# Kernel tuning notes

Measured on AMD Instinct MI355X. Metric: run time of the kernel, lower is better.

Reference implementation:

```python
import jax, jax.numpy as jnp
import numpy as np

N_SRC = 50000; N_DST = 50000; E = 800000
IN_NODE = 128; IN_EDGE = 16; OUT_NODE = 64; OUT_EDGE = 16; H = 4
LEAKY_SLOPE = 0.01  # F.leaky_relu default used inside dgl EGATConv


def setup_inputs() -> dict:
    key = jax.random.key(0)
    ks = jax.random.split(key, 11)
    return dict(
        nfeats=jax.random.normal(ks[0], (N_SRC, IN_NODE), jnp.float32),
        dst_feats=jax.random.normal(ks[1], (N_DST, IN_NODE), jnp.float32),
        reward=jax.random.uniform(ks[2], (E,), jnp.float32),
        src=jax.random.randint(ks[3], (E,), 0, N_SRC),
        dst=jax.random.randint(ks[4], (E,), 0, N_DST),
        W_ns=jax.random.normal(ks[5], (IN_NODE, H * OUT_NODE), jnp.float32) * 0.05,
        b_ns=jnp.zeros((H * OUT_NODE,), jnp.float32),
        W_ni=jax.random.normal(ks[6], (IN_NODE, H * OUT_EDGE), jnp.float32) * 0.05,
        W_nj=jax.random.normal(ks[7], (IN_NODE, H * OUT_EDGE), jnp.float32) * 0.05,
        W_fij=jax.random.normal(ks[8], (IN_EDGE, H * OUT_EDGE), jnp.float32) * 0.05,
        attn=jax.random.normal(ks[9], (H, OUT_EDGE), jnp.float32) * 0.05,
        b_e=jnp.zeros((H * OUT_EDGE,), jnp.float32),
    )


def reference(nfeats, dst_feats, reward, src, dst,
              W_ns, b_ns, W_ni, W_nj, W_fij, attn, b_e):
    # EGAT.forward with num_layers=1: efeats = reward repeated to IN_EDGE cols
    efeats = jnp.repeat(reward[:, None], IN_EDGE, axis=1)              # (E, Fe_in)
    # --- EGATConv ---
    f_ni = nfeats @ W_ni                                               # (Ns, H*Fe)
    f_nj = dst_feats @ W_nj                                            # (Nd, H*Fe)
    f_out = f_ni[src] + f_nj[dst] + efeats @ W_fij + b_e               # (E, H*Fe)
    f_out = jax.nn.leaky_relu(f_out, LEAKY_SLOPE).reshape(E, H, OUT_EDGE)
    e = jnp.einsum('ehf,hf->eh', f_out, attn)                          # (E, H)
    # edge softmax over incoming edges of each dst node (stable)
    m = jax.ops.segment_max(e, dst, num_segments=N_DST)                # (Nd, H)
    a = jnp.exp(e - m[dst])
    s = jax.ops.segment_sum(a, dst, num_segments=N_DST)                # (Nd, H)
    a = a / jnp.where(s > 0, s, 1.0)[dst]                              # (E, H)
    # weighted aggregation of projected src features
    h_src = (nfeats @ W_ns + b_ns).reshape(N_SRC, H, OUT_NODE)
    msg = h_src[src] * a[:, :, None]                                   # (E, H, Fn)
    h_out = jax.ops.segment_sum(msg, dst, num_segments=N_DST)          # (Nd, H, Fn)
    # wrapper: mean over heads then ReLU
    return jax.nn.relu(h_out.mean(axis=1))                             # (Nd, Fn)
```

## Files before the change

kernel.cpp:

```cpp
#include <hip/hip_runtime.h>

#define IN_NODE 128
#define OUT_NODE 64
#define NHEAD 4
#define HN 256
#define HE 64
#define LEAKY 0.01f

typedef __attribute__((ext_vector_type(8))) short bf16x8;
typedef __attribute__((ext_vector_type(4))) float f32x4;

__device__ __forceinline__ float bf2f(unsigned short u) {
    union { unsigned u; float f; } v; v.u = ((unsigned)u) << 16; return v.f;
}
__device__ __forceinline__ unsigned short f2bf(float x) {
    union { float f; unsigned u; } v; v.f = x;
    unsigned r = v.u + 0x7FFF + ((v.u >> 16) & 1);
    return (unsigned short)(r >> 16);
}
__device__ __forceinline__ bf16x8 cvt8(float4 a, float4 b) {
    bf16x8 r;
    r[0] = (short)f2bf(a.x); r[1] = (short)f2bf(a.y);
    r[2] = (short)f2bf(a.z); r[3] = (short)f2bf(a.w);
    r[4] = (short)f2bf(b.x); r[5] = (short)f2bf(b.y);
    r[6] = (short)f2bf(b.z); r[7] = (short)f2bf(b.w);
    return r;
}

__global__ void prep_hist(const float* __restrict__ W_fij,
                          const float* __restrict__ W_ni,
                          const float* __restrict__ W_ns,
                          const float* __restrict__ W_nj,
                          const int* __restrict__ dst,
                          float* __restrict__ wsum, unsigned short* __restrict__ WT,
                          int* __restrict__ cnt, int E) {
    int b = blockIdx.x;
    if (b == 0) {
        int k = threadIdx.x;
        if (k < 64) {
            float s = 0.f;
#pragma unroll
            for (int c = 0; c < 16; ++c) s += W_fij[c * 64 + k];
            wsum[k] = s;
        }
        return;
    }
    if (b <= 12) {
        int base = (b - 1) * 4096 + threadIdx.x;
#pragma unroll
        for (int i = 0; i < 16; ++i) {
            int idx = base + i * 256;
            int g   = idx >> 11;
            int rem = idx & 2047;
            int c   = rem >> 9;
            int l   = (rem >> 3) & 63;
            int j   = rem & 7;
            int nl  = l & 15;
            int k   = c * 32 + (l >> 4) * 8 + j;
            unsigned short v;
            if (g < 4)       v = f2bf(W_ni[k * 64  + g * 16 + nl]);
            else if (g < 20) v = f2bf(W_ns[k * 256 + (g - 4) * 16 + nl]);
            else             v = f2bf(W_nj[k * 64  + (g - 20) * 16 + nl]);
            WT[idx] = v;
        }
        return;
    }
    int i = (b - 13) * 256 + threadIdx.x;
    if (i < E) atomicAdd(&cnt[dst[i]], 1);
}

__global__ __launch_bounds__(256) void scan_all(const int* __restrict__ cnt,
                                                int* __restrict__ row_ptr,
                                                int* __restrict__ partials,
                                                int* __restrict__ flags,
                                                int n, int E, int nb) {
    __shared__ int sums[256];
    __shared__ int s_base;
    int tid = threadIdx.x, b = blockIdx.x;
    int base = b * 1024;
    int v[4]; int tsum = 0;
#pragma unroll
    for (int j = 0; j < 4; ++j) {
        int idx = base + tid * 4 + j;
        v[j] = (idx < n) ? cnt[idx] : 0;
        tsum += v[j];
    }
    sums[tid] = tsum;
    __syncthreads();
    for (int off = 1; off < 256; off <<= 1) {
        int x = (tid >= off) ? sums[tid - off] : 0;
        __syncthreads();
        sums[tid] += x;
        __syncthreads();
    }
    if (tid == 255) {
        __hip_atomic_store(&partials[b], sums[255], __ATOMIC_RELAXED, __HIP_MEMORY_SCOPE_AGENT);
        __hip_atomic_store(&flags[b], 1, __ATOMIC_RELEASE, __HIP_MEMORY_SCOPE_AGENT);
    }
    if (tid < 64) {
        int val = 0;
        if (tid < nb) {
            while (__hip_atomic_load(&flags[tid], __ATOMIC_ACQUIRE, __HIP_MEMORY_SCOPE_AGENT) == 0) {
                __builtin_amdgcn_s_sleep(1);
            }
            val = __hip_atomic_load(&partials[tid], __ATOMIC_RELAXED, __HIP_MEMORY_SCOPE_AGENT);
        }
#pragma unroll
        for (int o = 1; o < 64; o <<= 1) {
            int x = __shfl_up(val, o);
            if (tid >= o) val += x;
        }
        int off = (b > 0) ? __shfl(val, b - 1) : 0;
        if (tid == 0) s_base = off;
    }
    __syncthreads();
    int run = s_base + sums[tid] - tsum;
#pragma unroll
    for (int j = 0; j < 4; ++j) {
        int idx = base + tid * 4 + j;
        if (idx < n) row_ptr[idx] = run;
        run += v[j];
    }
    if (b == nb - 1 && tid == 0) row_ptr[n] = E;
}

template<int NG, int G0>
__device__ __forceinline__ void gemm_tile(
    const float* __restrict__ A, int rowBase, int M,
    const unsigned short* __restrict__ WB, const float* __restrict__ b_ns,
    unsigned short* __restrict__ f_ni, unsigned short* __restrict__ h_src,
    unsigned short* __restrict__ f_nj, unsigned short* As)
{
    const int t = threadIdx.x;
    const float4* A4 = reinterpret_cast<const float4*>(A);
#pragma unroll
    for (int j = 0; j < 4; ++j) {
        int gi = j * 256 + t;
        int r  = gi >> 4;
        int gr = rowBase + r; if (gr >= M) gr = M - 1;
        int fi = (gi & 15) * 2;
        float4 a0 = A4[(size_t)gr * 32 + fi];
        float4 a1 = A4[(size_t)gr * 32 + fi + 1];
        int byteoff = (gi * 16) ^ ((r & 7) << 4);
        *reinterpret_cast<bf16x8*>(reinterpret_cast<char*>(As) + byteoff) = cvt8(a0, a1);
    }
    __syncthreads();

    const int lane = t & 63, w = t >> 6;
    const int rw = rowBase + w * 16;
    if (rw >= M) return;
    const int m = lane & 15, q = lane >> 4;
    const int tr = w * 16 + m;

    f32x4 acc[NG] = {};
    const char* Asb = reinterpret_cast<const char*>(As);
#pragma unroll
    for (int c = 0; c < 4; ++c) {
        int gi  = tr * 16 + c * 4 + q;
        int off = (gi * 16) ^ ((tr & 7) << 4);
        bf16x8 af = *reinterpret_cast<const bf16x8*>(Asb + off);
#pragma unroll
        for (int g = 0; g < NG; ++g) {
            bf16x8 bf = *reinterpret_cast<const bf16x8*>(
                WB + (size_t)(((G0 + g) * 4 + c) * 64 + lane) * 8);
            acc[g] = __builtin_amdgcn_mfma_f32_16x16x32_bf16(af, bf, acc[g], 0, 0, 0);
        }
    }

#pragma unroll
    for (int g = 0; g < NG; ++g) {
        const int ga = G0 + g;
        unsigned short* C; int N, colBase; const float* bias = nullptr;
        if (ga < 4)       { C = f_ni;  N = 64;  colBase = ga * 16; }
        else if (ga < 20) { C = h_src; N = 256; colBase = (ga - 4) * 16; bias = b_ns; }
        else              { C = f_nj;  N = 64;  colBase = (ga - 20) * 16; }
        int col = colBase + m;
        float bv = bias ? bias[col] : 0.f;
#pragma unroll
        for (int rr = 0; rr < 4; ++rr) {
            int orow = rw + q * 4 + rr;
            if (orow < M) C[(size_t)orow * N + col] = f2bf(acc[g][rr] + bv);
        }
    }
}

__global__ __launch_bounds__(256) void mega(
    const float* __restrict__ nfeats, const float* __restrict__ dst_feats,
    const unsigned short* __restrict__ WT, const float* __restrict__ b_ns,
    const int* __restrict__ src, const int* __restrict__ dst,
    const float* __restrict__ reward, const int* __restrict__ row_ptr,
    int* __restrict__ cnt,
    unsigned short* __restrict__ f_ni, unsigned short* __restrict__ h_src,
    unsigned short* __restrict__ f_nj, int2* __restrict__ sr_s,
    int Ns, int Nd, int E, int nBlkNf, int nBlkDj, int nScatter)
{
    __shared__ __align__(16) unsigned short As[64 * 128];
    const int g = blockIdx.x / 3, r = blockIdx.x % 3;
    if (r == 0) {
        if (g < nBlkNf) {
            gemm_tile<20, 0>(nfeats, g * 64, Ns, WT, b_ns, f_ni, h_src, f_nj, As);
        } else if (g < nBlkNf + nBlkDj) {
            gemm_tile<4, 20>(dst_feats, (g - nBlkNf) * 64, Nd, WT, b_ns, f_ni, h_src, f_nj, As);
        }
        return;
    }
    const int sb = g * 2 + (r - 1);
    if (sb >= nScatter) return;
    int i = sb * 256 + threadIdx.x;
    if (i >= E) return;
    int d = dst[i];
    int pos = row_ptr[d] + atomicSub(&cnt[d], 1) - 1;
    sr_s[pos] = make_int2(src[i], __float_as_int(reward[i]));
}

__global__ __launch_bounds__(256) void fused_agg(
    const unsigned short* __restrict__ f_ni, const unsigned short* __restrict__ f_nj,
    const unsigned short* __restrict__ h_src, const int2* __restrict__ sr_s,
    const int* __restrict__ row_ptr,
    const float* __restrict__ wsum, const float* __restrict__ b_e,
    const float* __restrict__ attn, float* __restrict__ out, int Nd)
{
    const int wv = threadIdx.x >> 6, lane = threadIdx.x & 63;
    const int d = blockIdx.x * 4 + wv;
    if (d >= Nd) return;
    const int l = lane & 15, sub = lane >> 4;
    const int beg = row_ptr[d];
    const int end = row_ptr[d + 1];
    const int hsel = (lane >> 4) << 2;

    ushort4 uj = *reinterpret_cast<const ushort4*>(f_nj + (size_t)d * HE + 4 * l);
    float4 fnj = { bf2f(uj.x), bf2f(uj.y), bf2f(uj.z), bf2f(uj.w) };
    float4 ws = *reinterpret_cast<const float4*>(wsum + 4 * l);
    float4 be = *reinterpret_cast<const float4*>(b_e + 4 * l);
    float4 at = *reinterpret_cast<const float4*>(attn + 4 * l);

    float den = 0.f;
    float a0 = 0.f, a1 = 0.f, a2 = 0.f, a3 = 0.f;

    const int deg = end - beg;
    const int nfull = deg & ~3;

    for (int base = beg; base < beg + nfull; base += 4) {
        int2 sr = sr_s[base + sub];
        int sn = sr.x;
        float r = __int_as_float(sr.y);
        ushort4 ui = *reinterpret_cast<const ushort4*>(f_ni + (size_t)sn * HE + 4 * l);
        float t, v;
        v = bf2f(ui.x) + fnj.x + r * ws.x + be.x; v = (v >= 0.f) ? v : LEAKY * v; t  = v * at.x;
        v = bf2f(ui.y) + fnj.y + r * ws.y + be.y; v = (v >= 0.f) ? v : LEAKY * v; t += v * at.y;
        v = bf2f(ui.z) + fnj.z + r * ws.z + be.z; v = (v >= 0.f) ? v : LEAKY * v; t += v * at.z;
        v = bf2f(ui.w) + fnj.w + r * ws.w + be.w; v = (v >= 0.f) ? v : LEAKY * v; t += v * at.w;
        t += __shfl_xor(t, 1);
        t += __shfl_xor(t, 2);
        float ev = __expf(t);
        den += ev;
#pragma unroll
        for (int e = 0; e < 4; ++e) {
            float w  = __shfl(ev, e * 16 + hsel);
            int   sa = __shfl(sn, e * 16);
            ushort4 u = *reinterpret_cast<const ushort4*>(h_src + (size_t)sa * HN + lane * 4);
            a0 = fmaf(w, bf2f(u.x), a0);
            a1 = fmaf(w, bf2f(u.y), a1);
            a2 = fmaf(w, bf2f(u.z), a2);
            a3 = fmaf(w, bf2f(u.w), a3);
        }
    }

    const int rem = deg & 3;
    if (rem) {
        int base = beg + nfull;
        int slot = base + sub;
        float ev = 0.f; int sn = 0;
        if (sub < rem) {
            int2 sr = sr_s[slot];
            sn = sr.x;
            float r = __int_as_float(sr.y);
            ushort4 ui = *reinterpret_cast<const ushort4*>(f_ni + (size_t)sn * HE + 4 * l);
            float t, v;
            v = bf2f(ui.x) + fnj.x + r * ws.x + be.x; v = (v >= 0.f) ? v : LEAKY * v; t  = v * at.x;
            v = bf2f(ui.y) + fnj.y + r * ws.y + be.y; v = (v >= 0.f) ? v : LEAKY * v; t += v * at.y;
            v = bf2f(ui.z) + fnj.z + r * ws.z + be.z; v = (v >= 0.f) ? v : LEAKY * v; t += v * at.z;
            v = bf2f(ui.w) + fnj.w + r * ws.w + be.w; v = (v >= 0.f) ? v : LEAKY * v; t += v * at.w;
            t += __shfl_xor(t, 1);
            t += __shfl_xor(t, 2);
            ev = __expf(t);
            den += ev;
        }
        for (int e = 0; e < rem; ++e) {
            float w  = __shfl(ev, e * 16 + hsel);
            int   sa = __shfl(sn, e * 16);
            ushort4 u = *reinterpret_cast<const ushort4*>(h_src + (size_t)sa * HN + lane * 4);
            a0 = fmaf(w, bf2f(u.x), a0);
            a1 = fmaf(w, bf2f(u.y), a1);
            a2 = fmaf(w, bf2f(u.z), a2);
            a3 = fmaf(w, bf2f(u.w), a3);
        }
    }

    den += __shfl_xor(den, 16);
    den += __shfl_xor(den, 32);
    float dh = __shfl(den, hsel);
    float invh = (dh > 0.f) ? 1.f / dh : 0.f;
    a0 *= invh; a1 *= invh; a2 *= invh; a3 *= invh;

    a0 += __shfl_xor(a0, 16); a0 += __shfl_xor(a0, 32);
    a1 += __shfl_xor(a1, 16); a1 += __shfl_xor(a1, 32);
    a2 += __shfl_xor(a2, 16); a2 += __shfl_xor(a2, 32);
    a3 += __shfl_xor(a3, 16); a3 += __shfl_xor(a3, 32);
    if (lane < 16) {
        float4 o = { fmaxf(a0 * 0.25f, 0.f), fmaxf(a1 * 0.25f, 0.f),
                     fmaxf(a2 * 0.25f, 0.f), fmaxf(a3 * 0.25f, 0.f) };
        *reinterpret_cast<float4*>(out + (size_t)d * OUT_NODE + lane * 4) = o;
    }
}

static inline char* align256(char* p) {
    return (char*)(((uintptr_t)p + 255) & ~(uintptr_t)255);
}

extern "C" void kernel_launch(void* const* d_in, const int* in_sizes, int n_in,
                              void* d_out, int out_size, void* d_ws, size_t ws_size,
                              hipStream_t stream) {
    const float* nfeats    = (const float*)d_in[0];
    const float* dst_feats = (const float*)d_in[1];
    const float* reward    = (const float*)d_in[2];
    const int*   src       = (const int*)d_in[3];
    const int*   dst       = (const int*)d_in[4];
    const float* W_ns      = (const float*)d_in[5];
    const float* b_ns      = (const float*)d_in[6];
    const float* W_ni      = (const float*)d_in[7];
    const float* W_nj      = (const float*)d_in[8];
    const float* W_fij     = (const float*)d_in[9];
    const float* attn      = (const float*)d_in[10];
    const float* b_e       = (const float*)d_in[11];
    float* out = (float*)d_out;

    const int Ns = in_sizes[0] / IN_NODE;
    const int Nd = in_sizes[1] / IN_NODE;
    const int E  = in_sizes[2];

    char* ws = (char*)d_ws;
    unsigned short* f_ni  = (unsigned short*)ws; ws = align256(ws + (size_t)Ns * HE * 2);
    unsigned short* f_nj  = (unsigned short*)ws; ws = align256(ws + (size_t)Nd * HE * 2);
    unsigned short* h_src = (unsigned short*)ws; ws = align256(ws + (size_t)Ns * HN * 2);
    unsigned short* WT    = (unsigned short*)ws; ws = align256(ws + 49152 * 2);
    float* wsum    = (float*)ws; ws = align256(ws + HE * 4);
    int*   cnt     = (int*)ws;
    int*   flags   = cnt + Nd;   ws = align256(ws + (size_t)(Nd + 64) * 4);
    int*   row_ptr = (int*)ws;   ws = align256(ws + (size_t)(Nd + 1) * 4);
    int*   partials= (int*)ws;   ws = align256(ws + 256 * 4);
    int2*  sr_s    = (int2*)ws;  ws = align256(ws + (size_t)E * 8);

    hipMemsetAsync(cnt, 0, (size_t)(Nd + 64) * 4, stream);

    prep_hist<<<13 + (E + 255) / 256, 256, 0, stream>>>(
        W_fij, W_ni, W_ns, W_nj, dst, wsum, WT, cnt, E);

    int nb = (Nd + 1023) / 1024;
    scan_all<<<nb, 256, 0, stream>>>(cnt, row_ptr, partials, flags, Nd, E, nb);

    int nBlkNf = (Ns + 63) / 64;
    int nBlkDj = (Nd + 63) / 64;
    int nG = nBlkNf + nBlkDj;
    int nScatter = (E + 255) / 256;
    int nGroups = (nG > (nScatter + 1) / 2) ? nG : (nScatter + 1) / 2;
    mega<<<nGroups * 3, 256, 0, stream>>>(
        nfeats, dst_feats, WT, b_ns, src, dst, reward, row_ptr, cnt,
        f_ni, h_src, f_nj, sr_s, Ns, Nd, E, nBlkNf, nBlkDj, nScatter);

    fused_agg<<<(Nd + 3) / 4, 256, 0, stream>>>(
        f_ni, f_nj, h_src, sr_s, row_ptr, wsum, b_e, attn, out, Nd);
}
```

Measured before the change: 278.1 us.

## Software-pipeline edge gathers and restructure per-edge-group aggregation in fused_agg

Reworks the aggregation loop so each 16-lane group handles its own edge and gathers the full 256-wide h_src row for it, instead of broadcasting each edge's source index across the wave. It also prefetches the next edge's index, f_ni and h_src rows one iteration ahead and folds the remainder edges into the main loop through clamped indices and a validity mask. Softmax normalisation is applied per head at the end. The intent is to hide gather latency and remove the serial shuffle-then-load chain, at the cost of more registers, which may lower occupancy.

Result: no change. 273.0 us (-1.8%).

```diff
diff --git a/kernel.cpp b/kernel.cpp
--- a/kernel.cpp
+++ b/kernel.cpp
@@ -224,92 +224,115 @@
     const int d = blockIdx.x * 4 + wv;
     if (d >= Nd) return;
     const int l = lane & 15, sub = lane >> 4;
+
     const int beg = row_ptr[d];
     const int end = row_ptr[d + 1];
-    const int hsel = (lane >> 4) << 2;
+    const int deg = end - beg;
+
+    if (deg <= 0) {
+        if (lane < 16) {
+            float4 z = {0.f, 0.f, 0.f, 0.f};
+            *reinterpret_cast<float4*>(out + (size_t)d * OUT_NODE + lane * 4) = z;
+        }
+        return;
+    }
 
     ushort4 uj = *reinterpret_cast<const ushort4*>(f_nj + (size_t)d * HE + 4 * l);
-    float4 fnj = { bf2f(uj.x), bf2f(uj.y), bf2f(uj.z), bf2f(uj.w) };
     float4 ws = *reinterpret_cast<const float4*>(wsum + 4 * l);
     float4 be = *reinterpret_cast<const float4*>(b_e + 4 * l);
     float4 at = *reinterpret_cast<const float4*>(attn + 4 * l);
+    float4 bb = { bf2f(uj.x) + be.x, bf2f(uj.y) + be.y,
+                  bf2f(uj.z) + be.z, bf2f(uj.w) + be.w };
+
+    const int nq = (deg + 3) >> 2;
+    const int last = end - 1;
 
     float den = 0.f;
-    float a0 = 0.f, a1 = 0.f, a2 = 0.f, a3 = 0.f;
-
-    const int deg = end - beg;
-    const int nfull = deg & ~3;
-
-    for (int base = beg; base < beg + nfull; base += 4) {
-        int2 sr = sr_s[base + sub];
-        int sn = sr.x;
-        float r = __int_as_float(sr.y);
-        ushort4 ui = *reinterpret_cast<const ushort4*>(f_ni + (size_t)sn * HE + 4 * l);
-        float t, v;
-        v = bf2f(ui.x) + fnj.x + r * ws.x + be.x; v = (v >= 0.f) ? v : LEAKY * v; t  = v * at.x;
-        v = bf2f(ui.y) + fnj.y + r * ws.y + be.y; v = (v >= 0.f) ? v : LEAKY * v; t += v * at.y;
-        v = bf2f(ui.z) + fnj.z + r * ws.z + be.z; v = (v >= 0.f) ? v : LEAKY * v; t += v * at.z;
-        v = bf2f(ui.w) + fnj.w + r * ws.w + be.w; v = (v >= 0.f) ? v : LEAKY * v; t += v * at.w;
+    f32x4 ac0 = {}, ac1 = {}, ac2 = {}, ac3 = {};
+
+#define LDSR(q) ({ int qq = ((q) < nq) ? (q) : (nq - 1);                 \
+                   int slot = beg + qq * 4 + sub;                        \
+                   if (slot > last) slot = last;                         \
+                   sr_s[slot]; })
+
+    int2 srA = LDSR(0);
+    int2 srB = LDSR(1);
+    const unsigned short* pA = f_ni + (size_t)srA.x * HE + 4 * l;
+    ushort4 uiA = *reinterpret_cast<const ushort4*>(pA);
+    const unsigned short* hA = h_src + (size_t)srA.x * HN + 4 * l;
+    ushort4 uA0 = *reinterpret_cast<const ushort4*>(hA);
+    ushort4 uA1 = *reinterpret_cast<const ushort4*>(hA + 64);
+    ushort4 uA2 = *reinterpret_cast<const ushort4*>(hA + 128);
+    ushort4 uA3 = *reinterpret_cast<const ushort4*>(hA + 192);
+
+    for (int k = 0; k < nq; ++k) {
+        int2 srC = LDSR(k + 2);
+        const unsigned short* pB = f_ni + (size_t)srB.x * HE + 4 * l;
+        ushort4 uiB = *reinterpret_cast<const ushort4*>(pB);
+        const unsigned short* hB = h_src + (size_t)srB.x * HN + 4 * l;
+        ushort4 uB0 = *reinterpret_cast<const ushort4*>(hB);
+        ushort4 uB1 = *reinterpret_cast<const ushort4*>(hB + 64);
+        ushort4 uB2 = *reinterpret_cast<const ushort4*>(hB + 128);
+        ushort4 uB3 = *reinterpret_cast<const ushort4*>(hB + 192);
+
+        float r = __int_as_float(srA.y);
+        float v, t;
+        v = bf2f(uiA.x) + fmaf(r, ws.x, bb.x); v = fmaxf(v, LEAKY * v); t  = v * at.x;
+        v = bf2f(uiA.y) + fmaf(r, ws.y, bb.y); v = fmaxf(v, LEAKY * v); t = fmaf(v, at.y, t);
+        v = bf2f(uiA.z) + fmaf(r, ws.z, bb.z); v = fmaxf(v, LEAKY * v); t = fmaf(v, at.z, t);
+        v = bf2f(uiA.w) + fmaf(r, ws.w, bb.w); v = fmaxf(v, LEAKY * v); t = fmaf(v, at.w, t);
         t += __shfl_xor(t, 1);
         t += __shfl_xor(t, 2);
-        float ev = __expf(t);
+        bool valid = (beg + k * 4 + sub) < end;
+        float ev = valid ? __expf(t) : 0.f;
         den += ev;
-#pragma unroll
-        for (int e = 0; e < 4; ++e) {
-            float w  = __shfl(ev, e * 16 + hsel);
-            int   sa = __shfl(sn, e * 16);
-            ushort4 u = *reinterpret_cast<const ushort4*>(h_src + (size_t)sa * HN + lane * 4);
-            a0 = fmaf(w, bf2f(u.x), a0);
-            a1 = fmaf(w, bf2f(u.y), a1);
-            a2 = fmaf(w, bf2f(u.z), a2);
-            a3 = fmaf(w, bf2f(u.w), a3);
-        }
-    }
-
-    const int rem = deg & 3;
-    if (rem) {
-        int base = beg + nfull;
-        int slot = base + sub;
-        float ev = 0.f; int sn = 0;
-        if (sub < rem) {
-            int2 sr = sr_s[slot];
-            sn = sr.x;
-            float r = __int_as_float(sr.y);
-            ushort4 ui = *reinterpret_cast<const ushort4*>(f_ni + (size_t)sn * HE + 4 * l);
-            float t, v;
-            v = bf2f(ui.x) + fnj.x + r * ws.x + be.x; v = (v >= 0.f) ? v : LEAKY * v; t  = v * at.x;
-            v = bf2f(ui.y) + fnj.y + r * ws.y + be.y; v = (v >= 0.f) ? v : LEAKY * v; t += v * at.y;
-            v = bf2f(ui.z) + fnj.z + r * ws.z + be.z; v = (v >= 0.f) ? v : LEAKY * v; t += v * at.z;
-            v = bf2f(ui.w) + fnj.w + r * ws.w + be.w; v = (v >= 0.f) ? v : LEAKY * v; t += v * at.w;
-            t += __shfl_xor(t, 1);
-            t += __shfl_xor(t, 2);
-            ev = __expf(t);
-            den += ev;
-        }
-        for (int e = 0; e < rem; ++e) {
-            float w  = __shfl(ev, e * 16 + hsel);
-            int   sa = __shfl(sn, e * 16);
-            ushort4 u = *reinterpret_cast<const ushort4*>(h_src + (size_t)sa * HN + lane * 4);
-            a0 = fmaf(w, bf2f(u.x), a0);
-            a1 = fmaf(w, bf2f(u.y), a1);
-            a2 = fmaf(w, bf2f(u.z), a2);
-            a3 = fmaf(w, bf2f(u.w), a3);
-        }
-    }
+        float w0 = __shfl(ev, (lane & 48));
+        float w1 = __shfl(ev, (lane & 48) + 4);
+        float w2 = __shfl(ev, (lane & 48) + 8);
+        float w3 = __shfl(ev, (lane & 48) + 12);
+        ac0[0] = fmaf(w0, bf2f(uA0.x), ac0[0]);
+        ac0[1] = fmaf(w0, bf2f(uA0.y), ac0[1]);
+        ac0[2] = fmaf(w0, bf2f(uA0.z), ac0[2]);
+        ac0[3] = fmaf(w0, bf2f(uA0.w), ac0[3]);
+        ac1[0] = fmaf(w1, bf2f(uA1.x), ac1[0]);
+        ac1[1] = fmaf(w1, bf2f(uA1.y), ac1[1]);
+        ac1[2] = fmaf(w1, bf2f(uA1.z), ac1[2]);
+        ac1[3] = fmaf(w1, bf2f(uA1.w), ac1[3]);
+        ac2[0] = fmaf(w2, bf2f(uA2.x), ac2[0]);
+        ac2[1] = fmaf(w2, bf2f(uA2.y), ac2[1]);
+        ac2[2] = fmaf(w2, bf2f(uA2.z), ac2[2]);
+        ac2[3] = fmaf(w2, bf2f(uA2.w), ac2[3]);
+        ac3[0] = fmaf(w3, bf2f(uA3.x), ac3[0]);
+        ac3[1] = fmaf(w3, bf2f(uA3.y), ac3[1]);
+        ac3[2] = fmaf(w3, bf2f(uA3.z), ac3[2]);
+        ac3[3] = fmaf(w3, bf2f(uA3.w), ac3[3]);
+
+        srA = srB; srB = srC;
+        uiA = uiB;
+        uA0 = uB0; uA1 = uB1; uA2 = uB2; uA3 = uB3;
+    }
+#undef LDSR
 
     den += __shfl_xor(den, 16);
     den += __shfl_xor(den, 32);
-    float dh = __shfl(den, hsel);
-    float invh = (dh > 0.f) ? 1.f / dh : 0.f;
-    a0 *= invh; a1 *= invh; a2 *= invh; a3 *= invh;
-
-    a0 += __shfl_xor(a0, 16); a0 += __shfl_xor(a0, 32);
-    a1 += __shfl_xor(a1, 16); a1 += __shfl_xor(a1, 32);
-    a2 += __shfl_xor(a2, 16); a2 += __shfl_xor(a2, 32);
-    a3 += __shfl_xor(a3, 16); a3 += __shfl_xor(a3, 32);
+    float d0 = __shfl(den, 0), d1 = __shfl(den, 4);
+    float d2 = __shfl(den, 8), d3 = __shfl(den, 12);
+    float i0 = (d0 > 0.f) ? 0.25f / d0 : 0.f;
+    float i1 = (d1 > 0.f) ? 0.25f / d1 : 0.f;
+    float i2 = (d2 > 0.f) ? 0.25f / d2 : 0.f;
+    float i3 = (d3 > 0.f) ? 0.25f / d3 : 0.f;
+
+    float o0 = fmaf(ac3[0], i3, fmaf(ac2[0], i2, fmaf(ac1[0], i1, ac0[0] * i0)));
+    float o1 = fmaf(ac3[1], i3, fmaf(ac2[1], i2, fmaf(ac1[1], i1, ac0[1] * i0)));
+    float o2 = fmaf(ac3[2], i3, fmaf(ac2[2], i2, fmaf(ac1[2], i1, ac0[2] * i0)));
+    float o3 = fmaf(ac3[3], i3, fmaf(ac2[3], i2, fmaf(ac1[3], i1, ac0[3] * i0)));
+    o0 += __shfl_xor(o0, 16); o0 += __shfl_xor(o0, 32);
+    o1 += __shfl_xor(o1, 16); o1 += __shfl_xor(o1, 32);
+    o2 += __shfl_xor(o2, 16); o2 += __shfl_xor(o2, 32);
+    o3 += __shfl_xor(o3, 16); o3 += __shfl_xor(o3, 32);
     if (lane < 16) {
-        float4 o = { fmaxf(a0 * 0.25f, 0.f), fmaxf(a1 * 0.25f, 0.f),
-                     fmaxf(a2 * 0.25f, 0.f), fmaxf(a3 * 0.25f, 0.f) };
+        float4 o = { fmaxf(o0, 0.f), fmaxf(o1, 0.f),
+                     fmaxf(o2, 0.f), fmaxf(o3, 0.f) };
         *reinterpret_cast<float4*>(out + (size_t)d * OUT_NODE + lane * 4) = o;
     }
 }
```

## Restructure edge aggregation with multi-node waves, software-pipelined gathers, and LDS head reduction

Applied to the files above, without the earlier changes.

The fused aggregation kernel now gives each wavefront 8 destination nodes instead of one. Edge gathers are software-pipelined two iterations ahead, and each lane handles a full edge's 16-element h_src slice with wide loads, where before four shuffled per-edge loads were used. Packed float2 math handles the bf16 conversion, leaky-relu and accumulation, and the head and sub-group reduction goes through LDS instead of cross-lane shuffles. The aim is to hide gather latency and cut shuffle and instruction overhead. The cost is more registers, which may lower occupancy, and coarser load balancing across nodes.

Measured after the change: 279.4 us. Within noise of the previous version (+0.5%).

```diff
diff --git a/kernel.cpp b/kernel.cpp
--- a/kernel.cpp
+++ b/kernel.cpp
@@ -6,9 +6,11 @@
 #define HN 256
 #define HE 64
 #define LEAKY 0.01f
+#define DPW 8
 
 typedef __attribute__((ext_vector_type(8))) short bf16x8;
 typedef __attribute__((ext_vector_type(4))) float f32x4;
+typedef __attribute__((ext_vector_type(2))) float f32x2;
 
 __device__ __forceinline__ float bf2f(unsigned short u) {
     union { unsigned u; float f; } v; v.u = ((unsigned)u) << 16; return v.f;
@@ -25,6 +27,11 @@
     r[4] = (short)f2bf(b.x); r[5] = (short)f2bf(b.y);
     r[6] = (short)f2bf(b.z); r[7] = (short)f2bf(b.w);
     return r;
+}
+__device__ __forceinline__ f32x2 bfcvt2(unsigned d) {
+    union { unsigned u; float f; } lo, hi;
+    lo.u = d << 16; hi.u = d & 0xFFFF0000u;
+    f32x2 r; r.x = lo.f; r.y = hi.f; return r;
 }
 
 __global__ void prep_hist(const float* __restrict__ W_fij,
@@ -213,6 +220,18 @@
     sr_s[pos] = make_int2(src[i], __float_as_int(reward[i]));
 }
 
+struct G { uint2 ui; uint4 h0; uint4 h1; };
+__device__ __forceinline__ G gatherE(const unsigned short* __restrict__ f_ni,
+                                     const unsigned short* __restrict__ h_src,
+                                     int sn, int ll, int hq) {
+    G g;
+    g.ui = *reinterpret_cast<const uint2*>(f_ni + (size_t)sn * HE + 4 * ll);
+    const unsigned short* hp = h_src + (size_t)sn * HN + hq;
+    g.h0 = *reinterpret_cast<const uint4*>(hp);
+    g.h1 = *reinterpret_cast<const uint4*>(hp + 8);
+    return g;
+}
+
 __global__ __launch_bounds__(256) void fused_agg(
     const unsigned short* __restrict__ f_ni, const unsigned short* __restrict__ f_nj,
     const unsigned short* __restrict__ h_src, const int2* __restrict__ sr_s,
@@ -220,97 +239,106 @@
     const float* __restrict__ wsum, const float* __restrict__ b_e,
     const float* __restrict__ attn, float* __restrict__ out, int Nd)
 {
+    __shared__ float red[4][1024];
     const int wv = threadIdx.x >> 6, lane = threadIdx.x & 63;
-    const int d = blockIdx.x * 4 + wv;
-    if (d >= Nd) return;
-    const int l = lane & 15, sub = lane >> 4;
-    const int beg = row_ptr[d];
-    const int end = row_ptr[d + 1];
-    const int hsel = (lane >> 4) << 2;
-
-    ushort4 uj = *reinterpret_cast<const ushort4*>(f_nj + (size_t)d * HE + 4 * l);
-    float4 fnj = { bf2f(uj.x), bf2f(uj.y), bf2f(uj.z), bf2f(uj.w) };
-    float4 ws = *reinterpret_cast<const float4*>(wsum + 4 * l);
-    float4 be = *reinterpret_cast<const float4*>(b_e + 4 * l);
-    float4 at = *reinterpret_cast<const float4*>(attn + 4 * l);
-
-    float den = 0.f;
-    float a0 = 0.f, a1 = 0.f, a2 = 0.f, a3 = 0.f;
-
-    const int deg = end - beg;
-    const int nfull = deg & ~3;
-
-    for (int base = beg; base < beg + nfull; base += 4) {
-        int2 sr = sr_s[base + sub];
-        int sn = sr.x;
-        float r = __int_as_float(sr.y);
-        ushort4 ui = *reinterpret_cast<const ushort4*>(f_ni + (size_t)sn * HE + 4 * l);
-        float t, v;
-        v = bf2f(ui.x) + fnj.x + r * ws.x + be.x; v = (v >= 0.f) ? v : LEAKY * v; t  = v * at.x;
-        v = bf2f(ui.y) + fnj.y + r * ws.y + be.y; v = (v >= 0.f) ? v : LEAKY * v; t += v * at.y;
-        v = bf2f(ui.z) + fnj.z + r * ws.z + be.z; v = (v >= 0.f) ? v : LEAKY * v; t += v * at.z;
-        v = bf2f(ui.w) + fnj.w + r * ws.w + be.w; v = (v >= 0.f) ? v : LEAKY * v; t += v * at.w;
-        t += __shfl_xor(t, 1);
-        t += __shfl_xor(t, 2);
-        float ev = __expf(t);
-        den += ev;
-#pragma unroll
-        for (int e = 0; e < 4; ++e) {
-            float w  = __shfl(ev, e * 16 + hsel);
-            int   sa = __shfl(sn, e * 16);
-            ushort4 u = *reinterpret_cast<const ushort4*>(h_src + (size_t)sa * HN + lane * 4);
-            a0 = fmaf(w, bf2f(u.x), a0);
-            a1 = fmaf(w, bf2f(u.y), a1);
-            a2 = fmaf(w, bf2f(u.z), a2);
-            a3 = fmaf(w, bf2f(u.w), a3);
-        }
-    }
-
-    const int rem = deg & 3;
-    if (rem) {
-        int base = beg + nfull;
-        int slot = base + sub;
-        float ev = 0.f; int sn = 0;
-        if (sub < rem) {
-            int2 sr = sr_s[slot];
-            sn = sr.x;
-            float r = __int_as_float(sr.y);
-            ushort4 ui = *reinterpret_cast<const ushort4*>(f_ni + (size_t)sn * HE + 4 * l);
-            float t, v;
-            v = bf2f(ui.x) + fnj.x + r * ws.x + be.x; v = (v >= 0.f) ? v : LEAKY * v; t  = v * at.x;
-            v = bf2f(ui.y) + fnj.y + r * ws.y + be.y; v = (v >= 0.f) ? v : LEAKY * v; t += v * at.y;
-            v = bf2f(ui.z) + fnj.z + r * ws.z + be.z; v = (v >= 0.f) ? v : LEAKY * v; t += v * at.z;
-            v = bf2f(ui.w) + fnj.w + r * ws.w + be.w; v = (v >= 0.f) ? v : LEAKY * v; t += v * at.w;
-            t += __shfl_xor(t, 1);
-            t += __shfl_xor(t, 2);
-            ev = __expf(t);
-            den += ev;
-        }
-        for (int e = 0; e < rem; ++e) {
-            float w  = __shfl(ev, e * 16 + hsel);
-            int   sa = __shfl(sn, e * 16);
-            ushort4 u = *reinterpret_cast<const ushort4*>(h_src + (size_t)sa * HN + lane * 4);
-            a0 = fmaf(w, bf2f(u.x), a0);
-            a1 = fmaf(w, bf2f(u.y), a1);
-            a2 = fmaf(w, bf2f(u.z), a2);
-            a3 = fmaf(w, bf2f(u.w), a3);
-        }
-    }
-
-    den += __shfl_xor(den, 16);
-    den += __shfl_xor(den, 32);
-    float dh = __shfl(den, hsel);
-    float invh = (dh > 0.f) ? 1.f / dh : 0.f;
-    a0 *= invh; a1 *= invh; a2 *= invh; a3 *= invh;
-
-    a0 += __shfl_xor(a0, 16); a0 += __shfl_xor(a0, 32);
-    a1 += __shfl_xor(a1, 16); a1 += __shfl_xor(a1, 32);
-    a2 += __shfl_xor(a2, 16); a2 += __shfl_xor(a2, 32);
-    a3 += __shfl_xor(a3, 16); a3 += __shfl_xor(a3, 32);
-    if (lane < 16) {
-        float4 o = { fmaxf(a0 * 0.25f, 0.f), fmaxf(a1 * 0.25f, 0.f),
-                     fmaxf(a2 * 0.25f, 0.f), fmaxf(a3 * 0.25f, 0.f) };
-        *reinterpret_cast<float4*>(out + (size_t)d * OUT_NODE + lane * 4) = o;
+    const int gw = blockIdx.x * 4 + wv;
+    const int ll = lane & 15, sub = lane >> 4;
+    const int hq = ((lane >> 2) & 3) * 64 + (lane & 3) * 16;
+
+    int d0 = gw * DPW;
+    if (d0 >= Nd) return;
+    int d1 = d0 + DPW; if (d1 > Nd) d1 = Nd;
+
+    float4 wsv = *reinterpret_cast<const float4*>(wsum + 4 * ll);
+    float4 bev = *reinterpret_cast<const float4*>(b_e + 4 * ll);
+    float4 atv = *reinterpret_cast<const float4*>(attn + 4 * ll);
+    f32x2 ws01 = {wsv.x, wsv.y}, ws23 = {wsv.z, wsv.w};
+    f32x2 at01 = {atv.x, atv.y}, at23 = {atv.z, atv.w};
+    const f32x2 lk2 = {LEAKY, LEAKY};
+
+    int nextBeg = row_ptr[d0];
+    for (int d = d0; d < d1; ++d) {
+        const int beg = nextBeg;
+        const int end = row_ptr[d + 1];
+        nextBeg = end;
+        const int deg = end - beg;
+
+        float den = 0.f;
+        f32x2 a0 = {}, a1 = {}, a2 = {}, a3 = {}, a4 = {}, a5 = {}, a6 = {}, a7 = {};
+
+        if (deg > 0) {
+            uint2 uj = *reinterpret_cast<const uint2*>(f_nj + (size_t)d * HE + 4 * ll);
+            f32x2 bb01 = bfcvt2(uj.x) + (f32x2){bev.x, bev.y};
+            f32x2 bb23 = bfcvt2(uj.y) + (f32x2){bev.z, bev.w};
+            const int nq = (deg + 3) >> 2;
+            const int last = end - 1;
+
+#define LDSR(q) ({ int qq_ = ((q) < nq) ? (q) : (nq - 1);                 \
+                   int slot_ = beg + qq_ * 4 + sub;                       \
+                   if (slot_ > last) slot_ = last;                        \
+                   sr_s[slot_]; })
+
+#define COMPUTE(sr, gg, kq) do {                                          \
+    float r_ = __int_as_float((sr).y);                                    \
+    f32x2 r2_ = {r_, r_};                                                 \
+    f32x2 v01_ = bfcvt2((gg).ui.x) + r2_ * ws01 + bb01;                   \
+    f32x2 v23_ = bfcvt2((gg).ui.y) + r2_ * ws23 + bb23;                   \
+    v01_ = __builtin_elementwise_max(v01_, v01_ * lk2);                   \
+    v23_ = __builtin_elementwise_max(v23_, v23_ * lk2);                   \
+    f32x2 t2_ = v01_ * at01 + v23_ * at23;                                \
+    float t_ = t2_.x + t2_.y;                                             \
+    t_ += __shfl_xor(t_, 1);                                              \
+    t_ += __shfl_xor(t_, 2);                                              \
+    float ev_ = ((beg + (kq) * 4 + sub) < end) ? __expf(t_) : 0.f;        \
+    den += ev_;                                                           \
+    f32x2 ev2_ = {ev_, ev_};                                              \
+    a0 += bfcvt2((gg).h0.x) * ev2_;                                       \
+    a1 += bfcvt2((gg).h0.y) * ev2_;                                       \
+    a2 += bfcvt2((gg).h0.z) * ev2_;                                       \
+    a3 += bfcvt2((gg).h0.w) * ev2_;                                       \
+    a4 += bfcvt2((gg).h1.x) * ev2_;                                       \
+    a5 += bfcvt2((gg).h1.y) * ev2_;                                       \
+    a6 += bfcvt2((gg).h1.z) * ev2_;                                       \
+    a7 += bfcvt2((gg).h1.w) * ev2_;                                       \
+} while (0)
+
+            int2 sr0 = LDSR(0), sr1 = LDSR(1), sr2 = LDSR(2);
+            G gA = gatherE(f_ni, h_src, sr0.x, ll, hq);
+            G gB = gatherE(f_ni, h_src, sr1.x, ll, hq);
+            for (int k = 0; k < nq; k += 2) {
+                int2 sr3 = LDSR(k + 3);
+                G gC = gatherE(f_ni, h_src, sr2.x, ll, hq);
+                COMPUTE(sr0, gA, k);
+                int2 sr4 = LDSR(k + 4);
+                G gD = gatherE(f_ni, h_src, sr3.x, ll, hq);
+                if (k + 1 < nq) COMPUTE(sr1, gB, k + 1);
+                sr0 = sr2; sr1 = sr3; sr2 = sr4; gA = gC; gB = gD;
+            }
+#undef COMPUTE
+#undef LDSR
+        }
+
+        den += __shfl_xor(den, 16);
+        den += __shfl_xor(den, 32);
+        float sc = (den > 0.f) ? 0.25f / den : 0.f;
+        float* wr = &red[wv][sub * 256 + hq];
+        float4 s0 = {a0.x * sc, a0.y * sc, a1.x * sc, a1.y * sc};
+        float4 s1 = {a2.x * sc, a2.y * sc, a3.x * sc, a3.y * sc};
+        float4 s2 = {a4.x * sc, a4.y * sc, a5.x * sc, a5.y * sc};
+        float4 s3 = {a6.x * sc, a6.y * sc, a7.x * sc, a7.y * sc};
+        *reinterpret_cast<float4*>(wr)      = s0;
+        *reinterpret_cast<float4*>(wr + 4)  = s1;
+        *reinterpret_cast<float4*>(wr + 8)  = s2;
+        *reinterpret_cast<float4*>(wr + 12) = s3;
+        asm volatile("s_waitcnt lgkmcnt(0)" ::: "memory");
+        float ssum = 0.f;
+        const float* rd = &red[wv][lane];
+#pragma unroll
+        for (int s = 0; s < 4; ++s)
+#pragma unroll
+            for (int h = 0; h < 4; ++h)
+                ssum += rd[s * 256 + h * 64];
+        out[(size_t)d * OUT_NODE + lane] = fmaxf(ssum, 0.f);
     }
 }
 
@@ -368,6 +396,8 @@
         nfeats, dst_feats, WT, b_ns, src, dst, reward, row_ptr, cnt,
         f_ni, h_src, f_nj, sr_s, Ns, Nd, E, nBlkNf, nBlkDj, nScatter);
 
-    fused_agg<<<(Nd + 3) / 4, 256, 0, stream>>>(
+    int nWavesF = (Nd + DPW - 1) / DPW;
+    int nBlocksF = (nWavesF + 3) / 4;
+    fused_agg<<<nBlocksF, 256, 0, stream>>>(
         f_ni, f_nj, h_src, sr_s, row_ptr, wsum, b_e, attn, out, Nd);
 }
```
